# Kernel optimization log

Measured on AMD Instinct MI355X. Metric: run time of the kernel, lower is better.

The kernel has to match this reference:

```python
import jax, jax.numpy as jnp
import numpy as np

DIM = 1024
H = 16
HD = DIM // H  # 64
SCALE = HD ** -0.5
EPS = 1e-5


def setup_inputs() -> dict:
    key = jax.random.key(0)
    ks = jax.random.split(key, 8)
    B, N = 2, 2048
    x = jax.random.normal(ks[0], (B, N, DIM), dtype=jnp.float32)
    qkv_w = jax.random.normal(ks[1], (5 * DIM, DIM), dtype=jnp.float32) * (DIM ** -0.5)
    proj_w = jax.random.normal(ks[2], (DIM, DIM), dtype=jnp.float32) * (DIM ** -0.5)
    proj_b = jnp.zeros((DIM,), dtype=jnp.float32)
    lambda_q1 = jax.random.normal(ks[3], (HD,), dtype=jnp.float32) * 0.1
    lambda_k1 = jax.random.normal(ks[4], (HD,), dtype=jnp.float32) * 0.1
    lambda_q2 = jax.random.normal(ks[5], (HD,), dtype=jnp.float32) * 0.1
    lambda_k2 = jax.random.normal(ks[6], (HD,), dtype=jnp.float32) * 0.1
    return {"x": x, "qkv_w": qkv_w, "proj_w": proj_w, "proj_b": proj_b,
            "lambda_q1": lambda_q1, "lambda_k1": lambda_k1,
            "lambda_q2": lambda_q2, "lambda_k2": lambda_k2}


def reference(x, qkv_w, proj_w, proj_b, lambda_q1, lambda_k1, lambda_q2, lambda_k2):
    B, N, C = x.shape
    # qkv projection -> (5, B, H, N, hd)
    qkv = jnp.einsum('bnc,fc->bnf', x, qkv_w).reshape(B, N, 5, H, HD)
    qkv = jnp.transpose(qkv, (2, 0, 3, 1, 4))
    q1, q2, k1, k2, v = qkv[0], qkv[1], qkv[2], qkv[3], qkv[4]
    # dual attention score matrices (B, H, N, N)
    attn1 = jax.nn.softmax(jnp.einsum('bhqd,bhkd->bhqk', q1, k1) * SCALE, axis=-1)
    attn2 = jax.nn.softmax(jnp.einsum('bhqd,bhkd->bhqk', q2, k2) * SCALE, axis=-1)
    lambda_full = (jnp.exp(jnp.sum(lambda_q1 * lambda_k1))
                   - jnp.exp(jnp.sum(lambda_q2 * lambda_k2)) + 0.8)
    attn = attn1 - lambda_full * attn2
    out = jnp.einsum('bhqk,bhkd->bhqd', attn, v)  # (B,H,N,hd)
    out = jnp.transpose(out, (0, 2, 1, 3)).reshape(B, N, C)
    # RMSNorm (no affine) over last dim, then fixed scale (1 - 0.8)
    out = out * jax.lax.rsqrt(jnp.mean(out * out, axis=-1, keepdims=True) + EPS)
    out = out * (1.0 - 0.8)
    return jnp.einsum('bnc,oc->bno', out, proj_w) + proj_b
```

## Files before the change

### kernel.cpp

```cpp
#include <hip/hip_runtime.h>
#include <hip/hip_bf16.h>

#define SEQ   2048
#define BATCH 2
#define NHEAD 16
#define HDIM  64
#define CDIM  1024
#define QKV_F 5120
#define SCALE 0.125f
#define EPSV  1e-5f

typedef __bf16 bf16;
typedef __bf16 bf16x8 __attribute__((ext_vector_type(8)));
typedef float  f32x4  __attribute__((ext_vector_type(4)));
typedef float  f32x16 __attribute__((ext_vector_type(16)));

#define MFMA16(a, b, c) __builtin_amdgcn_mfma_f32_16x16x32_bf16(a, b, c, 0, 0, 0)
#define MFMA32(a, b, c) __builtin_amdgcn_mfma_f32_32x32x16_bf16(a, b, c, 0, 0, 0)

__device__ __forceinline__ unsigned pkbf(float a, float b) {
    union { bf16 h[2]; unsigned u; } t;
    t.h[0] = (bf16)a; t.h[1] = (bf16)b;
    return t.u;
}
__device__ __forceinline__ unsigned short bfbits(float a) {
    union { bf16 h; unsigned short u; } t;
    t.h = (bf16)a;
    return t.u;
}

template <int EPI>
__global__ __launch_bounds__(256) void gemm_bt(
    const float* __restrict__ A, const float* __restrict__ Bw,
    const float* __restrict__ bias,
    bf16* __restrict__ outq, float* __restrict__ outp,
    int M, int Nn, int K)
{
    __shared__ __align__(16) bf16 As[128][72];
    __shared__ __align__(16) bf16 Bs[128][72];

    const int tid  = threadIdx.x;
    const int lane = tid & 63;
    const int wave = tid >> 6;
    const int wr = wave >> 1, wc = wave & 1;
    const int g = lane >> 4, fr = lane & 15;
    const int m0 = blockIdx.y * 128;
    const int n0 = blockIdx.x * 128;

    f32x4 acc[4][4];
#pragma unroll
    for (int m = 0; m < 4; ++m)
#pragma unroll
        for (int n = 0; n < 4; ++n) acc[m][n] = f32x4{0.f, 0.f, 0.f, 0.f};

    const int nkt = K >> 6;
    for (int kt = 0; kt < nkt; ++kt) {
        const int k0 = kt << 6;
        __syncthreads();
#pragma unroll
        for (int it = 0; it < 4; ++it) {
            int idx = it * 256 + tid;
            int row = idx >> 3;
            int c8  = (idx & 7) << 3;
            {
                const float* gp = A + (size_t)(m0 + row) * K + k0 + c8;
                float4 u = *(const float4*)gp;
                float4 v = *(const float4*)(gp + 4);
                bf16x8 t;
                t[0] = (bf16)u.x; t[1] = (bf16)u.y; t[2] = (bf16)u.z; t[3] = (bf16)u.w;
                t[4] = (bf16)v.x; t[5] = (bf16)v.y; t[6] = (bf16)v.z; t[7] = (bf16)v.w;
                *(bf16x8*)(&As[row][c8]) = t;
            }
            {
                const float* gp = Bw + (size_t)(n0 + row) * K + k0 + c8;
                float4 u = *(const float4*)gp;
                float4 v = *(const float4*)(gp + 4);
                bf16x8 t;
                t[0] = (bf16)u.x; t[1] = (bf16)u.y; t[2] = (bf16)u.z; t[3] = (bf16)u.w;
                t[4] = (bf16)v.x; t[5] = (bf16)v.y; t[6] = (bf16)v.z; t[7] = (bf16)v.w;
                *(bf16x8*)(&Bs[row][c8]) = t;
            }
        }
        __syncthreads();
#pragma unroll
        for (int ks = 0; ks < 2; ++ks) {
            bf16x8 af[4], bfr[4];
#pragma unroll
            for (int m = 0; m < 4; ++m)
                af[m] = *(const bf16x8*)(&As[wr * 64 + m * 16 + fr][ks * 32 + g * 8]);
#pragma unroll
            for (int n = 0; n < 4; ++n)
                bfr[n] = *(const bf16x8*)(&Bs[wc * 64 + n * 16 + fr][ks * 32 + g * 8]);
#pragma unroll
            for (int m = 0; m < 4; ++m)
#pragma unroll
                for (int n = 0; n < 4; ++n)
                    acc[m][n] = MFMA16(af[m], bfr[n], acc[m][n]);
        }
    }

#pragma unroll
    for (int m = 0; m < 4; ++m) {
#pragma unroll
        for (int n = 0; n < 4; ++n) {
            const int row0 = m0 + wr * 64 + m * 16 + g * 4;
            const int col  = n0 + wc * 64 + n * 16 + fr;
            if (EPI == 0) {
                const int bb = row0 >> 11, nn = row0 & (SEQ - 1);
                const int sI = col >> 10, rem = col & (CDIM - 1);
                const int hh = rem >> 6, dd = rem & 63;
                const size_t base = ((size_t)((sI * BATCH + bb) * NHEAD + hh)) << 17;
                if (sI == 4) {
                    ushort4 u;
                    u.x = bfbits(acc[m][n][0]);
                    u.y = bfbits(acc[m][n][1]);
                    u.z = bfbits(acc[m][n][2]);
                    u.w = bfbits(acc[m][n][3]);
                    *(ushort4*)(outq + base + ((size_t)dd << 11) + nn) = u;
                } else {
                    const float sc = (sI < 2) ? SCALE : 1.f;
#pragma unroll
                    for (int r = 0; r < 4; ++r)
                        outq[base + ((size_t)(nn + r) << 6) + dd] = (bf16)(acc[m][n][r] * sc);
                }
            } else {
#pragma unroll
                for (int r = 0; r < 4; ++r)
                    outp[(size_t)(row0 + r) * Nn + col] = acc[m][n][r] + bias[col];
            }
        }
    }
}

__device__ __forceinline__ void attn_state(
    const char* __restrict__ Ks, const bf16x8* qf, const bf16x8 (*vf)[2],
    int lq, int hi, int s32,
    f32x16& oa, f32x16& ob, float& mS, float& lS)
{
    f32x16 s;
#pragma unroll
    for (int r = 0; r < 16; ++r) s[r] = 0.f;
    const int krow = s32 * 32 + lq;
    const int ksw  = (krow & 7) << 4;
#pragma unroll
    for (int ks = 0; ks < 4; ++ks) {
        bf16x8 kf = *(const bf16x8*)(Ks + krow * 128 + ((ks * 32 + hi * 16) ^ ksw));
        s = MFMA32(kf, qf[ks], s);
    }
    float pm = s[0];
#pragma unroll
    for (int r = 1; r < 16; ++r) pm = fmaxf(pm, s[r]);
    pm = fmaxf(pm, __shfl_xor(pm, 32));
    if (!__all(pm <= mS + 8.f)) {
        float mn = fmaxf(mS, pm);
        float alpha = __expf(mS - mn);
        lS *= alpha;
        oa *= alpha;
        ob *= alpha;
        mS = mn;
    }
    float p[16];
    float rs = 0.f;
#pragma unroll
    for (int r = 0; r < 16; ++r) { p[r] = __expf(s[r] - mS); rs += p[r]; }
    rs += __shfl_xor(rs, 32);
    lS += rs;
#pragma unroll
    for (int s16 = 0; s16 < 2; ++s16) {
        unsigned X = pkbf(p[s16 * 8 + 0], p[s16 * 8 + 1]);
        unsigned Z = pkbf(p[s16 * 8 + 2], p[s16 * 8 + 3]);
        unsigned Y = pkbf(p[s16 * 8 + 4], p[s16 * 8 + 5]);
        unsigned W = pkbf(p[s16 * 8 + 6], p[s16 * 8 + 7]);
        auto xy = __builtin_amdgcn_permlane32_swap(X, Y, false, false);
        auto zw = __builtin_amdgcn_permlane32_swap(Z, W, false, false);
        union { unsigned u[4]; bf16x8 v; } pf;
        pf.u[0] = xy[0]; pf.u[1] = zw[0]; pf.u[2] = xy[1]; pf.u[3] = zw[1];
        oa = MFMA32(vf[0][s16], pf.v, oa);
        ob = MFMA32(vf[1][s16], pf.v, ob);
    }
}

__global__ __launch_bounds__(512, 2) void diff_attn(
    const bf16* __restrict__ qkv,
    const float* __restrict__ lq1, const float* __restrict__ lk1,
    const float* __restrict__ lq2, const float* __restrict__ lk2,
    float* __restrict__ attn_out)
{
    __shared__ __align__(16) char K1s[64 * 128];
    __shared__ __align__(16) char K2s[64 * 128];
    __shared__ __align__(16) char Vts[64 * 128];

    const int tid = threadIdx.x;
    const int lane = tid & 63, wave = tid >> 6;
    const int lq = lane & 31, hi = lane >> 5;
    const int bh = blockIdx.y, b = bh >> 4, h = bh & 15;
    const int q0w = blockIdx.x * 256 + wave * 32;

    float ls1 = 0.f, ls2 = 0.f;
    for (int i = 0; i < HDIM; ++i) { ls1 += lq1[i] * lk1[i]; ls2 += lq2[i] * lk2[i]; }
    const float lam = __expf(ls1) - __expf(ls2) + 0.8f;

    const size_t HS = (size_t)SEQ * HDIM;
    const char* q1p = (const char*)(qkv + ((size_t)((0 * BATCH + b) * NHEAD + h)) * HS);
    const char* q2p = (const char*)(qkv + ((size_t)((1 * BATCH + b) * NHEAD + h)) * HS);
    const char* k1p = (const char*)(qkv + ((size_t)((2 * BATCH + b) * NHEAD + h)) * HS);
    const char* k2p = (const char*)(qkv + ((size_t)((3 * BATCH + b) * NHEAD + h)) * HS);
    const char* vtp = (const char*)(qkv + ((size_t)((4 * BATCH + b) * NHEAD + h)) * HS);

    bf16x8 qf1[4], qf2[4];
#pragma unroll
    for (int ks = 0; ks < 4; ++ks) {
        qf1[ks] = *(const bf16x8*)(q1p + (size_t)(q0w + lq) * 128 + ks * 32 + hi * 16);
        qf2[ks] = *(const bf16x8*)(q2p + (size_t)(q0w + lq) * 128 + ks * 32 + hi * 16);
    }

    f32x16 o1a, o1b, o2a, o2b;
#pragma unroll
    for (int r = 0; r < 16; ++r) { o1a[r] = 0.f; o1b[r] = 0.f; o2a[r] = 0.f; o2b[r] = 0.f; }
    float m1 = -1e30f, l1 = 0.f, m2 = -1e30f, l2 = 0.f;

    const int srow = tid >> 3;
    const int sc   = (tid & 7) << 4;
    const int swc  = sc ^ ((srow & 7) << 4);

    for (int kt = 0; kt < SEQ / 64; ++kt) {
        __syncthreads();
        uint4 ka = *(const uint4*)(k1p + (size_t)(kt * 64 + srow) * 128 + sc);
        uint4 kb = *(const uint4*)(k2p + (size_t)(kt * 64 + srow) * 128 + sc);
        uint4 vv = *(const uint4*)(vtp + (size_t)srow * (SEQ * 2) + kt * 128 + sc);
        *(uint4*)(K1s + srow * 128 + swc) = ka;
        *(uint4*)(K2s + srow * 128 + swc) = kb;
        *(uint4*)(Vts + srow * 128 + swc) = vv;
        __syncthreads();

#pragma unroll
        for (int s32 = 0; s32 < 2; ++s32) {
            bf16x8 vf[2][2];
#pragma unroll
            for (int dt = 0; dt < 2; ++dt) {
                const int vrow = dt * 32 + lq;
                const int vsw  = (vrow & 7) << 4;
#pragma unroll
                for (int s16 = 0; s16 < 2; ++s16)
                    vf[dt][s16] = *(const bf16x8*)(Vts + vrow * 128 +
                                   ((s32 * 64 + s16 * 32 + hi * 16) ^ vsw));
            }
            attn_state(K1s, qf1, vf, lq, hi, s32, o1a, o1b, m1, l1);
            attn_state(K2s, qf2, vf, lq, hi, s32, o2a, o2b, m2, l2);
        }
    }

    const float i1 = 1.f / l1;
    const float i2 = lam / l2;
    const int nq = q0w + lq;
    float* op = attn_out + ((size_t)(b * SEQ + nq)) * CDIM + h * HDIM;
#pragma unroll
    for (int dt = 0; dt < 2; ++dt) {
        const f32x16& a1 = dt ? o1b : o1a;
        const f32x16& a2 = dt ? o2b : o2a;
#pragma unroll
        for (int rq = 0; rq < 4; ++rq) {
            const int d0 = dt * 32 + rq * 8 + hi * 4;
            float4 o;
            o.x = a1[rq * 4 + 0] * i1 - i2 * a2[rq * 4 + 0];
            o.y = a1[rq * 4 + 1] * i1 - i2 * a2[rq * 4 + 1];
            o.z = a1[rq * 4 + 2] * i1 - i2 * a2[rq * 4 + 2];
            o.w = a1[rq * 4 + 3] * i1 - i2 * a2[rq * 4 + 3];
            *(float4*)(op + d0) = o;
        }
    }
}

__global__ __launch_bounds__(256) void rmsnorm_inplace(float* __restrict__ io)
{
    __shared__ float red[4];
    const int row = blockIdx.x, tid = threadIdx.x;
    float4* p = (float4*)(io + (size_t)row * CDIM);
    float4 v = p[tid];
    float ss = v.x * v.x + v.y * v.y + v.z * v.z + v.w * v.w;
#pragma unroll
    for (int m = 1; m < 64; m <<= 1) ss += __shfl_xor(ss, m);
    if ((tid & 63) == 0) red[tid >> 6] = ss;
    __syncthreads();
    float tot = red[0] + red[1] + red[2] + red[3];
    float sc = rsqrtf(tot * (1.f / CDIM) + EPSV) * 0.2f;
    v.x *= sc; v.y *= sc; v.z *= sc; v.w *= sc;
    p[tid] = v;
}

extern "C" void kernel_launch(void* const* d_in, const int* in_sizes, int n_in,
                              void* d_out, int out_size, void* d_ws, size_t ws_size,
                              hipStream_t stream)
{
    (void)in_sizes; (void)n_in; (void)out_size; (void)ws_size;
    const float* x      = (const float*)d_in[0];
    const float* qkv_w  = (const float*)d_in[1];
    const float* proj_w = (const float*)d_in[2];
    const float* proj_b = (const float*)d_in[3];
    const float* lq1    = (const float*)d_in[4];
    const float* lk1    = (const float*)d_in[5];
    const float* lq2    = (const float*)d_in[6];
    const float* lk2    = (const float*)d_in[7];
    float* out = (float*)d_out;

    bf16*  qkv_t    = (bf16*)d_ws;
    float* attn_out = (float*)((char*)d_ws +
                       (size_t)5 * BATCH * NHEAD * SEQ * HDIM * sizeof(bf16));

    dim3 blk(256);
    gemm_bt<0><<<dim3(QKV_F / 128, (BATCH * SEQ) / 128), blk, 0, stream>>>(
        x, qkv_w, nullptr, qkv_t, nullptr, BATCH * SEQ, QKV_F, CDIM);
    diff_attn<<<dim3(SEQ / 256, BATCH * NHEAD), dim3(512), 0, stream>>>(
        qkv_t, lq1, lk1, lq2, lk2, attn_out);
    rmsnorm_inplace<<<dim3(BATCH * SEQ), blk, 0, stream>>>(attn_out);
    gemm_bt<1><<<dim3(CDIM / 128, (BATCH * SEQ) / 128), blk, 0, stream>>>(
        attn_out, proj_w, proj_b, nullptr, out, BATCH * SEQ, CDIM, CDIM);
}
```

Measured before the change: 251.0 us.

## Pre-convert GEMM operands to bf16, use direct global-to-LDS loads, exp2 softmax

```diff
diff --git a/kernel.cpp b/kernel.cpp
--- a/kernel.cpp
+++ b/kernel.cpp
@@ -8,9 +8,11 @@
 #define CDIM  1024
 #define QKV_F 5120
 #define SCALE 0.125f
+#define LOG2E 1.44269504f
 #define EPSV  1e-5f
 
 typedef __bf16 bf16;
+typedef __bf16 bf16x4 __attribute__((ext_vector_type(4)));
 typedef __bf16 bf16x8 __attribute__((ext_vector_type(8)));
 typedef float  f32x4  __attribute__((ext_vector_type(4)));
 typedef float  f32x16 __attribute__((ext_vector_type(16)));
@@ -28,16 +30,33 @@
     t.h = (bf16)a;
     return t.u;
 }
+__device__ __forceinline__ void gload16(const void* g, void* l) {
+    __builtin_amdgcn_global_load_lds(
+        (const __attribute__((address_space(1))) unsigned int*)g,
+        (__attribute__((address_space(3))) unsigned int*)l, 16, 0, 0);
+}
+
+__global__ __launch_bounds__(256) void cvt_bf16(
+    const float* __restrict__ s, bf16* __restrict__ d)
+{
+    const int i = (blockIdx.x * 256 + threadIdx.x) * 8;
+    float4 a = *(const float4*)(s + i);
+    float4 b = *(const float4*)(s + i + 4);
+    bf16x8 t;
+    t[0] = (bf16)a.x; t[1] = (bf16)a.y; t[2] = (bf16)a.z; t[3] = (bf16)a.w;
+    t[4] = (bf16)b.x; t[5] = (bf16)b.y; t[6] = (bf16)b.z; t[7] = (bf16)b.w;
+    *(bf16x8*)(d + i) = t;
+}
 
 template <int EPI>
-__global__ __launch_bounds__(256) void gemm_bt(
-    const float* __restrict__ A, const float* __restrict__ Bw,
+__global__ __launch_bounds__(256) void gemm_lds(
+    const bf16* __restrict__ A, const bf16* __restrict__ Bw,
     const float* __restrict__ bias,
     bf16* __restrict__ outq, float* __restrict__ outp,
     int M, int Nn, int K)
 {
-    __shared__ __align__(16) bf16 As[128][72];
-    __shared__ __align__(16) bf16 Bs[128][72];
+    __shared__ __align__(16) bf16 As[128 * 64];
+    __shared__ __align__(16) bf16 Bs[128 * 64];
 
     const int tid  = threadIdx.x;
     const int lane = tid & 63;
@@ -47,6 +66,9 @@
     const int m0 = blockIdx.y * 128;
     const int n0 = blockIdx.x * 128;
 
+    const int lrow = lane >> 3;
+    const int lcol = (lane & 7) << 3;
+
     f32x4 acc[4][4];
 #pragma unroll
     for (int m = 0; m < 4; ++m)
@@ -58,28 +80,11 @@
         const int k0 = kt << 6;
         __syncthreads();
 #pragma unroll
-        for (int it = 0; it < 4; ++it) {
-            int idx = it * 256 + tid;
-            int row = idx >> 3;
-            int c8  = (idx & 7) << 3;
-            {
-                const float* gp = A + (size_t)(m0 + row) * K + k0 + c8;
-                float4 u = *(const float4*)gp;
-                float4 v = *(const float4*)(gp + 4);
-                bf16x8 t;
-                t[0] = (bf16)u.x; t[1] = (bf16)u.y; t[2] = (bf16)u.z; t[3] = (bf16)u.w;
-                t[4] = (bf16)v.x; t[5] = (bf16)v.y; t[6] = (bf16)v.z; t[7] = (bf16)v.w;
-                *(bf16x8*)(&As[row][c8]) = t;
-            }
-            {
-                const float* gp = Bw + (size_t)(n0 + row) * K + k0 + c8;
-                float4 u = *(const float4*)gp;
-                float4 v = *(const float4*)(gp + 4);
-                bf16x8 t;
-                t[0] = (bf16)u.x; t[1] = (bf16)u.y; t[2] = (bf16)u.z; t[3] = (bf16)u.w;
-                t[4] = (bf16)v.x; t[5] = (bf16)v.y; t[6] = (bf16)v.z; t[7] = (bf16)v.w;
-                *(bf16x8*)(&Bs[row][c8]) = t;
-            }
+        for (int i = 0; i < 4; ++i) {
+            const int chunk = wave * 4 + i;
+            const int row = chunk * 8 + lrow;
+            gload16(A + (size_t)(m0 + row) * K + k0 + lcol, As + chunk * 512);
+            gload16(Bw + (size_t)(n0 + row) * K + k0 + lcol, Bs + chunk * 512);
         }
         __syncthreads();
 #pragma unroll
@@ -87,10 +92,10 @@
             bf16x8 af[4], bfr[4];
 #pragma unroll
             for (int m = 0; m < 4; ++m)
-                af[m] = *(const bf16x8*)(&As[wr * 64 + m * 16 + fr][ks * 32 + g * 8]);
+                af[m] = *(const bf16x8*)(As + (wr * 64 + m * 16 + fr) * 64 + ks * 32 + g * 8);
 #pragma unroll
             for (int n = 0; n < 4; ++n)
-                bfr[n] = *(const bf16x8*)(&Bs[wc * 64 + n * 16 + fr][ks * 32 + g * 8]);
+                bfr[n] = *(const bf16x8*)(Bs + (wc * 64 + n * 16 + fr) * 64 + ks * 32 + g * 8);
 #pragma unroll
             for (int m = 0; m < 4; ++m)
 #pragma unroll
@@ -118,7 +123,7 @@
                     u.w = bfbits(acc[m][n][3]);
                     *(ushort4*)(outq + base + ((size_t)dd << 11) + nn) = u;
                 } else {
-                    const float sc = (sI < 2) ? SCALE : 1.f;
+                    const float sc = (sI < 2) ? SCALE * LOG2E : 1.f;
 #pragma unroll
                     for (int r = 0; r < 4; ++r)
                         outq[base + ((size_t)(nn + r) << 6) + dd] = (bf16)(acc[m][n][r] * sc);
@@ -151,9 +156,9 @@
 #pragma unroll
     for (int r = 1; r < 16; ++r) pm = fmaxf(pm, s[r]);
     pm = fmaxf(pm, __shfl_xor(pm, 32));
-    if (!__all(pm <= mS + 8.f)) {
+    if (!__all(pm <= mS + 8.f * LOG2E)) {
         float mn = fmaxf(mS, pm);
-        float alpha = __expf(mS - mn);
+        float alpha = __builtin_amdgcn_exp2f(mS - mn);
         lS *= alpha;
         oa *= alpha;
         ob *= alpha;
@@ -162,7 +167,7 @@
     float p[16];
     float rs = 0.f;
 #pragma unroll
-    for (int r = 0; r < 16; ++r) { p[r] = __expf(s[r] - mS); rs += p[r]; }
+    for (int r = 0; r < 16; ++r) { p[r] = __builtin_amdgcn_exp2f(s[r] - mS); rs += p[r]; }
     rs += __shfl_xor(rs, 32);
     lS += rs;
 #pragma unroll
@@ -271,12 +276,12 @@
     }
 }
 
-__global__ __launch_bounds__(256) void rmsnorm_inplace(float* __restrict__ io)
+__global__ __launch_bounds__(256) void rmsnorm_bf16(
+    const float* __restrict__ in, bf16* __restrict__ out)
 {
     __shared__ float red[4];
     const int row = blockIdx.x, tid = threadIdx.x;
-    float4* p = (float4*)(io + (size_t)row * CDIM);
-    float4 v = p[tid];
+    const float4 v = ((const float4*)(in + (size_t)row * CDIM))[tid];
     float ss = v.x * v.x + v.y * v.y + v.z * v.z + v.w * v.w;
 #pragma unroll
     for (int m = 1; m < 64; m <<= 1) ss += __shfl_xor(ss, m);
@@ -284,8 +289,10 @@
     __syncthreads();
     float tot = red[0] + red[1] + red[2] + red[3];
     float sc = rsqrtf(tot * (1.f / CDIM) + EPSV) * 0.2f;
-    v.x *= sc; v.y *= sc; v.z *= sc; v.w *= sc;
-    p[tid] = v;
+    bf16x4 o;
+    o[0] = (bf16)(v.x * sc); o[1] = (bf16)(v.y * sc);
+    o[2] = (bf16)(v.z * sc); o[3] = (bf16)(v.w * sc);
+    ((bf16x4*)(out + (size_t)row * CDIM))[tid] = o;
 }
 
 extern "C" void kernel_launch(void* const* d_in, const int* in_sizes, int n_in,
@@ -303,16 +310,23 @@
     const float* lk2    = (const float*)d_in[7];
     float* out = (float*)d_out;
 
-    bf16*  qkv_t    = (bf16*)d_ws;
-    float* attn_out = (float*)((char*)d_ws +
-                       (size_t)5 * BATCH * NHEAD * SEQ * HDIM * sizeof(bf16));
+    char* ws = (char*)d_ws;
+    bf16*  qkv_t    = (bf16*)ws;
+    bf16*  attn_b   = (bf16*)ws;
+    float* attn_out = (float*)(ws + (size_t)40 * 1024 * 1024);
+    bf16*  x_b      = (bf16*)(ws + (size_t)40 * 1024 * 1024);
+    bf16*  qkvw_b   = (bf16*)(ws + (size_t)56 * 1024 * 1024);
+    bf16*  projw_b  = (bf16*)(ws + (size_t)66 * 1024 * 1024);
 
     dim3 blk(256);
-    gemm_bt<0><<<dim3(QKV_F / 128, (BATCH * SEQ) / 128), blk, 0, stream>>>(
-        x, qkv_w, nullptr, qkv_t, nullptr, BATCH * SEQ, QKV_F, CDIM);
+    cvt_bf16<<<dim3((BATCH * SEQ * CDIM) / 2048), blk, 0, stream>>>(x, x_b);
+    cvt_bf16<<<dim3((QKV_F * CDIM) / 2048), blk, 0, stream>>>(qkv_w, qkvw_b);
+    cvt_bf16<<<dim3((CDIM * CDIM) / 2048), blk, 0, stream>>>(proj_w, projw_b);
+    gemm_lds<0><<<dim3(QKV_F / 128, (BATCH * SEQ) / 128), blk, 0, stream>>>(
+        x_b, qkvw_b, nullptr, qkv_t, nullptr, BATCH * SEQ, QKV_F, CDIM);
     diff_attn<<<dim3(SEQ / 256, BATCH * NHEAD), dim3(512), 0, stream>>>(
         qkv_t, lq1, lk1, lq2, lk2, attn_out);
-    rmsnorm_inplace<<<dim3(BATCH * SEQ), blk, 0, stream>>>(attn_out);
-    gemm_bt<1><<<dim3(CDIM / 128, (BATCH * SEQ) / 128), blk, 0, stream>>>(
-        attn_out, proj_w, proj_b, nullptr, out, BATCH * SEQ, CDIM, CDIM);
-}
+    rmsnorm_bf16<<<dim3(BATCH * SEQ), blk, 0, stream>>>(attn_out, attn_b);
+    gemm_lds<1><<<dim3(CDIM / 128, (BATCH * SEQ) / 128), blk, 0, stream>>>(
+        attn_b, projw_b, proj_b, nullptr, out, BATCH * SEQ, CDIM, CDIM);
+}
```

Measured after the change: 226.4 us. 1.11x faster.
